# Kernel optimization log

Hardware: AMD Instinct MI355X
Metric: run time of the kernel (lower is better)

Reference implementation:

```python
import jax, jax.numpy as jnp
import numpy as np

NUM_HEADS = 16  # concat repeats the identical head output this many times


def setup_inputs() -> dict:
    key = jax.random.key(0)
    ks = jax.random.split(key, 6)
    B, S, E, D = 4, 4096, 1024, 64  # D = E // NUM_HEADS
    s_in = 1.0 / np.sqrt(E)
    return {
        "x": jax.random.normal(ks[0], (B, S, E), dtype=jnp.float32),
        "Wq": jax.random.normal(ks[1], (E, D), dtype=jnp.float32) * s_in,
        "bq": jnp.zeros((D,), dtype=jnp.float32),
        "Wk": jax.random.normal(ks[2], (E, D), dtype=jnp.float32) * s_in,
        "bk": jnp.zeros((D,), dtype=jnp.float32),
        "Wv": jax.random.normal(ks[3], (E, D), dtype=jnp.float32) * s_in,
        "bv": jnp.zeros((D,), dtype=jnp.float32),
        "Wo": jax.random.normal(ks[4], (E, E), dtype=jnp.float32) * s_in,
        "bo": jnp.zeros((E,), dtype=jnp.float32),
    }


def reference(x, Wq, bq, Wk, bk, Wv, bv, Wo, bo):
    # Single shared projection to head_dim (the torch code projects E -> E//H once).
    q = x @ Wq + bq          # [B,S,D]
    k = x @ Wk + bk          # [B,S,D]
    v = x @ Wv + bv          # [B,S,D]
    d = q.shape[-1]
    scale = 1.0 / jnp.sqrt(jnp.asarray(d, dtype=q.dtype))
    scores = jnp.einsum("bqd,bkd->bqk", q, k) * scale   # [B,S,S]
    attn = jax.nn.softmax(scores, axis=-1)
    ctx = jnp.einsum("bqk,bkd->bqd", attn, v)            # [B,S,D]
    # Every head computes the identical result; concat == tile along features.
    cat = jnp.tile(ctx, (1, 1, NUM_HEADS))               # [B,S,E]
    return cat @ Wo + bo
```

## Files before the change

kernel.cpp:

```cpp
#include <hip/hip_runtime.h>
#include <hip/hip_bf16.h>

#define BB 4
#define SS 4096
#define EE 1024
#define DD 64

typedef unsigned short u16;
typedef unsigned int   u32;
typedef __bf16 bf16_t;
typedef bf16_t bf16x2 __attribute__((ext_vector_type(2)));
typedef bf16_t bf16x8 __attribute__((ext_vector_type(8)));
typedef float  f32x4  __attribute__((ext_vector_type(4)));
typedef u32    u32x4  __attribute__((ext_vector_type(4)));

__device__ __forceinline__ u16 f2bf_hw(float f) {
    bf16_t b = (bf16_t)f;
    u16 u; __builtin_memcpy(&u, &b, 2);
    return u;
}
__device__ __forceinline__ void bfsplit(float v, u16& h, u16& l) {
    bf16_t hb = (bf16_t)v;
    float hf = (float)hb;
    __builtin_memcpy(&h, &hb, 2);
    bf16_t lb = (bf16_t)(v - hf);
    __builtin_memcpy(&l, &lb, 2);
}

__global__ __launch_bounds__(256) void prep_kernel(const float* __restrict__ Wq,
                                                   const float* __restrict__ Wk,
                                                   const float* __restrict__ Wv,
                                                   const float* __restrict__ Wo,
                                                   u16* __restrict__ Wt,
                                                   u16* __restrict__ WoTh,
                                                   u16* __restrict__ WoTl) {
    const int b = blockIdx.x;
    const int tid = threadIdx.x;
    if (b < 768) {
        int t = b * 256 + tid;
        int c = t >> 10, e = t & 1023;
        const float* W = (c < 64) ? Wq : (c < 128) ? Wk : Wv;
        Wt[c * 1024 + e] = f2bf_hw(W[e * 64 + (c & 63)]);
        return;
    }
    const int t = (b - 768) * 256 + tid;
    const int d = t >> 10, e = t & 1023;
    float s = 0.f;
    #pragma unroll
    for (int h = 0; h < 16; h++) s += Wo[(h * 64 + d) * 1024 + e];
    u16 hh, ll;
    bfsplit(s, hh, ll);
    WoTh[e * 64 + d] = hh;
    WoTl[e * 64 + d] = ll;
}

__global__ __launch_bounds__(256) void proj_kernel(const float* __restrict__ x,
                                                   const u16* __restrict__ Wtg,
                                                   const float* __restrict__ bq,
                                                   const float* __restrict__ bk,
                                                   const float* __restrict__ bv,
                                                   u16* __restrict__ Qg,
                                                   u16* __restrict__ Kg,
                                                   u16* __restrict__ Vtg) {
    __shared__ __align__(16) u16 xt[32 * 136];
    __shared__ __align__(16) u16 wts[192 * 136];

    const int tid  = threadIdx.x;
    const int w    = tid >> 6;
    const int lane = tid & 63;
    const int m    = lane & 15;
    const int quad = lane >> 4;
    const int r0   = blockIdx.x * 32;
    const int mt   = w & 1;
    const int ch   = w >> 1;

    f32x4 acc[6];
    #pragma unroll
    for (int i = 0; i < 6; i++) acc[i] = (f32x4){0.f, 0.f, 0.f, 0.f};

    f32x4 xr[4];
    u32x4 wr[12];

    auto preload = [&](int kb) {
        #pragma unroll
        for (int j = 0; j < 2; j++) {
            const int id = tid + j * 256, row = id >> 4, seg = id & 15;
            const float* src = x + (r0 + row) * 1024 + kb * 128 + seg * 8;
            xr[2 * j]     = *(const f32x4*)(src);
            xr[2 * j + 1] = *(const f32x4*)(src + 4);
        }
        #pragma unroll
        for (int j = 0; j < 12; j++) {
            const int id = tid + j * 256, row = id >> 4, seg = id & 15;
            wr[j] = *(const u32x4*)(Wtg + row * 1024 + kb * 128 + seg * 8);
        }
    };
    auto commit = [&]() {
        #pragma unroll
        for (int j = 0; j < 2; j++) {
            const int id = tid + j * 256, row = id >> 4, seg = id & 15;
            bf16x8 v;
            #pragma unroll
            for (int k = 0; k < 4; k++) {
                v[k]     = (bf16_t)xr[2 * j][k];
                v[4 + k] = (bf16_t)xr[2 * j + 1][k];
            }
            *(bf16x8*)(xt + row * 136 + seg * 8) = v;
        }
        #pragma unroll
        for (int j = 0; j < 12; j++) {
            const int id = tid + j * 256, row = id >> 4, seg = id & 15;
            *(u32x4*)(wts + row * 136 + seg * 8) = wr[j];
        }
    };

    preload(0);
    for (int kb = 0; kb < 8; kb++) {
        __syncthreads();
        commit();
        __syncthreads();
        if (kb < 7) preload(kb + 1);
        #pragma unroll
        for (int ks = 0; ks < 4; ks++) {
            bf16x8 a = *(const bf16x8*)(xt + (mt * 16 + m) * 136 + ks * 32 + quad * 8);
            #pragma unroll
            for (int c = 0; c < 6; c++) {
                bf16x8 b = *(const bf16x8*)(wts + (ch * 96 + c * 16 + m) * 136 + ks * 32 + quad * 8);
                acc[c] = __builtin_amdgcn_mfma_f32_16x16x32_bf16(a, b, acc[c], 0, 0, 0);
            }
        }
    }

    const int rbase = r0 + mt * 16 + quad * 4;
    #pragma unroll
    for (int c = 0; c < 6; c++) {
        const int col   = ch * 96 + c * 16 + m;
        const int which = col >> 6;
        const int d     = col & 63;
        const float bias = (which == 0 ? bq : which == 1 ? bk : bv)[d];
        #pragma unroll
        for (int r = 0; r < 4; r++) {
            const int row = rbase + r;
            float v = acc[c][r] + bias;
            if (which == 0) {
                Qg[row * 64 + d] = f2bf_hw(v * 0.125f);
            } else if (which == 1) {
                Kg[row * 64 + d] = f2bf_hw(v);
            } else {
                const int b = row >> 12, s = row & 4095;
                const int sp = (s & ~31) | ((s & 12) << 1) | (s & 3) | ((s >> 2) & 4);
                Vtg[(b * 64 + d) * 4096 + sp] = f2bf_hw(v);
            }
        }
    }
}

#define ATTN_LDS 73728
__global__ __launch_bounds__(512) void attn_kernel(const u16* __restrict__ Qg,
                                                   const u16* __restrict__ Kg,
                                                   const u16* __restrict__ Vtg,
                                                   float* __restrict__ ctxP,
                                                   float* __restrict__ liP) {
    extern __shared__ __align__(16) u16 smem[];

    const int tid  = threadIdx.x;
    const int w    = tid >> 6;
    const int lane = tid & 63;
    const int m    = lane & 15;
    const int quad = lane >> 4;
    const int kg   = w >> 1;
    const int qg   = w & 1;

    const int bi    = blockIdx.x;
    const int khalf = bi & 1;
    const int batch = (bi >> 1) & 3;
    const int qt    = bi >> 3;
    const int qrow0 = batch * 4096 + qt * 64;

    bf16x8 aq[2][2];
    #pragma unroll
    for (int s = 0; s < 2; s++) {
        const int qr = qrow0 + qg * 32 + s * 16 + m;
        aq[s][0] = *(const bf16x8*)(Qg + qr * 64 + quad * 8);
        aq[s][1] = *(const bf16x8*)(Qg + qr * 64 + 32 + quad * 8);
    }

    f32x4 acc[2][4];
    float li[2] = {0.f, 0.f};
    #pragma unroll
    for (int s = 0; s < 2; s++)
        #pragma unroll
        for (int c = 0; c < 4; c++) acc[s][c] = (f32x4){0.f, 0.f, 0.f, 0.f};

    const u16* Kbase = Kg + (batch * 4096 + khalf * 2048) * 64;
    const u16* Vbase = Vtg + batch * 64 * 4096 + khalf * 2048;

    const int krow = qg * 16 + (lane >> 3);
    const int kseg = lane & 7;
    const int kxor = (lane >> 3) & 7;
    const int vrow = qg * 32 + (lane >> 2);
    const int vseg = lane & 3;

    u32x4 kr[2], vr[2];
    auto preload = [&](int it) {
        const int k0 = it * 128 + kg * 32;
        #pragma unroll
        for (int i = 0; i < 2; i++) {
            kr[i] = *(const u32x4*)(Kbase + (k0 + krow + 8 * i) * 64 + kseg * 8);
            vr[i] = *(const u32x4*)(Vbase + (vrow + 16 * i) * 4096 + k0 + vseg * 8);
        }
    };
    auto commit = [&](u16* Kt, u16* Vt) {
        #pragma unroll
        for (int i = 0; i < 2; i++) {
            *(u32x4*)(Kt + (krow + 8 * i) * 64 + ((kseg ^ kxor) * 8)) = kr[i];
            *(u32x4*)(Vt + (vrow + 16 * i) * 40 + vseg * 8) = vr[i];
        }
    };

    const float LOG2E = 1.4426950408889634f;
    const float NC2   = -12.0f * 1.4426950408889634f;

    preload(0);
    {
        u16* base = smem + kg * 4608;
        commit(base, base + 2048);
    }
    __syncthreads();

    for (int it = 0; it < 16; it++) {
        const int cur = it & 1;
        u16* Kt = smem + cur * 18432 + kg * 4608;
        u16* Vt = Kt + 2048;

        if (it < 15) preload(it + 1);

        f32x4 sc[2][2];
        #pragma unroll
        for (int c = 0; c < 2; c++) {
            const int row = c * 16 + m;
            bf16x8 k0f = *(const bf16x8*)(Kt + row * 64 + ((quad ^ (m & 7)) * 8));
            bf16x8 k1f = *(const bf16x8*)(Kt + row * 64 + (((quad | 4) ^ (m & 7)) * 8));
            #pragma unroll
            for (int s = 0; s < 2; s++) {
                f32x4 t = __builtin_amdgcn_mfma_f32_16x16x32_bf16(k0f, aq[s][0], (f32x4){0.f,0.f,0.f,0.f}, 0, 0, 0);
                sc[s][c] = __builtin_amdgcn_mfma_f32_16x16x32_bf16(k1f, aq[s][1], t, 0, 0, 0);
            }
        }

        bf16x8 pa[2];
        #pragma unroll
        for (int s = 0; s < 2; s++) {
            float p[8];
            #pragma unroll
            for (int r = 0; r < 4; r++) {
                p[r]     = __builtin_exp2f(__builtin_fmaf(sc[s][0][r], LOG2E, NC2));
                p[4 + r] = __builtin_exp2f(__builtin_fmaf(sc[s][1][r], LOG2E, NC2));
            }
            li[s] += ((p[0] + p[1]) + (p[2] + p[3])) + ((p[4] + p[5]) + (p[6] + p[7]));
            #pragma unroll
            for (int j = 0; j < 8; j++) pa[s][j] = (bf16_t)p[j];
        }

        #pragma unroll
        for (int c = 0; c < 4; c++) {
            bf16x8 bv = *(const bf16x8*)(Vt + (c * 16 + m) * 40 + quad * 8);
            #pragma unroll
            for (int s = 0; s < 2; s++)
                acc[s][c] = __builtin_amdgcn_mfma_f32_16x16x32_bf16(pa[s], bv, acc[s][c], 0, 0, 0);
        }

        if (it < 15) {
            u16* Kn = smem + (cur ^ 1) * 18432 + kg * 4608;
            commit(Kn, Kn + 2048);
        }
        __syncthreads();
    }

    #pragma unroll
    for (int s = 0; s < 2; s++) {
        float v = li[s];
        v += __shfl_xor(v, 16);
        v += __shfl_xor(v, 32);
        li[s] = v;
    }

    float* mf = (float*)smem;
    float* cb = mf + w * 2208;
    #pragma unroll
    for (int s = 0; s < 2; s++)
        #pragma unroll
        for (int c = 0; c < 4; c++)
            #pragma unroll
            for (int r = 0; r < 4; r++)
                cb[(s * 16 + quad * 4 + r) * 68 + c * 16 + m] = acc[s][c][r];
    if (lane < 16) {
        #pragma unroll
        for (int s = 0; s < 2; s++) cb[2176 + s * 16 + m] = li[s];
    }
    __syncthreads();

    const int q  = tid >> 3;
    const int d0 = (tid & 7) * 8;
    const int qgq = q >> 5;
    const int ql  = q & 31;
    float L = 0.f;
    f32x4 o0 = (f32x4){0.f, 0.f, 0.f, 0.f};
    f32x4 o1 = (f32x4){0.f, 0.f, 0.f, 0.f};
    #pragma unroll
    for (int g = 0; g < 4; g++) {
        const float* c2 = mf + (g * 2 + qgq) * 2208;
        L  += c2[2176 + ql];
        o0 += *(const f32x4*)(c2 + ql * 68 + d0);
        o1 += *(const f32x4*)(c2 + ql * 68 + d0 + 4);
    }
    const int gr = khalf * 16384 + qrow0 + q;
    *(f32x4*)(ctxP + gr * 64 + d0)     = o0;
    *(f32x4*)(ctxP + gr * 64 + d0 + 4) = o1;
    if ((tid & 7) == 0) liP[gr] = L;
}

__global__ __launch_bounds__(256) void out_kernel(const float* __restrict__ ctxP,
                                                  const float* __restrict__ liP,
                                                  const u16* __restrict__ WoTh,
                                                  const u16* __restrict__ WoTl,
                                                  const float* __restrict__ bo,
                                                  float* __restrict__ out) {
    __shared__ __align__(16) u16 ldsH[64 * 72];
    __shared__ __align__(16) u16 ldsL[64 * 72];
    const int tid = threadIdx.x;
    const int r0  = (blockIdx.x >> 2) * 64;
    const int eb  = (blockIdx.x & 3) * 256;

    {
        const int q  = tid >> 2;
        const int dq = (tid & 3) * 16;
        const float inv = 1.0f / (liP[r0 + q] + liP[16384 + r0 + q]);
        const float* A = ctxP + (r0 + q) * 64 + dq;
        const float* B = ctxP + 16384 * 64 + (r0 + q) * 64 + dq;
        #pragma unroll
        for (int i = 0; i < 4; i++) {
            f32x4 a4 = *(const f32x4*)(A + i * 4);
            f32x4 b4 = *(const f32x4*)(B + i * 4);
            f32x4 o  = (a4 + b4) * inv;
            u16 h[4], l[4];
            #pragma unroll
            for (int k = 0; k < 4; k++) bfsplit(o[k], h[k], l[k]);
            u32 h0 = (u32)h[0] | ((u32)h[1] << 16);
            u32 h1 = (u32)h[2] | ((u32)h[3] << 16);
            u32 l0 = (u32)l[0] | ((u32)l[1] << 16);
            u32 l1 = (u32)l[2] | ((u32)l[3] << 16);
            const int off = q * 72 + dq + i * 4;
            *(u32*)(ldsH + off)     = h0;
            *(u32*)(ldsH + off + 2) = h1;
            *(u32*)(ldsL + off)     = l0;
            *(u32*)(ldsL + off + 2) = l1;
        }
    }
    __syncthreads();

    const int w    = tid >> 6;
    const int lane = tid & 63;
    const int m    = lane & 15;
    const int quad = lane >> 4;
    const int wr   = w >> 1;
    const int wc   = w & 1;

    bf16x8 aH[2][2], aL[2][2];
    #pragma unroll
    for (int rs = 0; rs < 2; rs++)
        #pragma unroll
        for (int ks = 0; ks < 2; ks++) {
            const int off = (wr * 32 + rs * 16 + m) * 72 + ks * 32 + quad * 8;
            aH[rs][ks] = *(const bf16x8*)(ldsH + off);
            aL[rs][ks] = *(const bf16x8*)(ldsL + off);
        }

    f32x4 acc[2][8];
    #pragma unroll
    for (int rs = 0; rs < 2; rs++)
        #pragma unroll
        for (int cs = 0; cs < 8; cs++) acc[rs][cs] = (f32x4){0.f, 0.f, 0.f, 0.f};

    #pragma unroll
    for (int cs = 0; cs < 8; cs++) {
        const int e = eb + wc * 128 + cs * 16 + m;
        bf16x8 bh0 = *(const bf16x8*)(WoTh + e * 64 + quad * 8);
        bf16x8 bh1 = *(const bf16x8*)(WoTh + e * 64 + 32 + quad * 8);
        bf16x8 bl0 = *(const bf16x8*)(WoTl + e * 64 + quad * 8);
        bf16x8 bl1 = *(const bf16x8*)(WoTl + e * 64 + 32 + quad * 8);
        #pragma unroll
        for (int rs = 0; rs < 2; rs++) {
            f32x4 t = acc[rs][cs];
            t = __builtin_amdgcn_mfma_f32_16x16x32_bf16(aH[rs][0], bh0, t, 0, 0, 0);
            t = __builtin_amdgcn_mfma_f32_16x16x32_bf16(aH[rs][1], bh1, t, 0, 0, 0);
            t = __builtin_amdgcn_mfma_f32_16x16x32_bf16(aL[rs][0], bh0, t, 0, 0, 0);
            t = __builtin_amdgcn_mfma_f32_16x16x32_bf16(aL[rs][1], bh1, t, 0, 0, 0);
            t = __builtin_amdgcn_mfma_f32_16x16x32_bf16(aH[rs][0], bl0, t, 0, 0, 0);
            t = __builtin_amdgcn_mfma_f32_16x16x32_bf16(aH[rs][1], bl1, t, 0, 0, 0);
            acc[rs][cs] = t;
        }
    }

    #pragma unroll
    for (int cs = 0; cs < 8; cs++) {
        const int e = eb + wc * 128 + cs * 16 + m;
        const float bov = bo[e];
        #pragma unroll
        for (int rs = 0; rs < 2; rs++) {
            const int row = r0 + wr * 32 + rs * 16 + quad * 4;
            #pragma unroll
            for (int r = 0; r < 4; r++)
                out[(row + r) * 1024 + e] = acc[rs][cs][r] + bov;
        }
    }
}

extern "C" void kernel_launch(void* const* d_in, const int* in_sizes, int n_in,
                              void* d_out, int out_size, void* d_ws, size_t ws_size,
                              hipStream_t stream) {
    const float* x  = (const float*)d_in[0];
    const float* Wq = (const float*)d_in[1];
    const float* bq = (const float*)d_in[2];
    const float* Wk = (const float*)d_in[3];
    const float* bk = (const float*)d_in[4];
    const float* Wv = (const float*)d_in[5];
    const float* bv = (const float*)d_in[6];
    const float* Wo = (const float*)d_in[7];
    const float* bo = (const float*)d_in[8];
    float* out = (float*)d_out;

    char* ws = (char*)d_ws;
    u16*   Wt   = (u16*)(ws);
    u16*   WoTh = (u16*)(ws + 393216);
    u16*   WoTl = (u16*)(ws + 524288);
    u16*   Qg   = (u16*)(ws + 655360);
    u16*   Kg   = (u16*)(ws + 2752512);
    u16*   Vtg  = (u16*)(ws + 4849664);
    float* ctxP = (float*)(ws + 6946816);
    float* liP  = (float*)(ws + 15335424);

    (void)hipFuncSetAttribute((const void*)attn_kernel,
                              hipFuncAttributeMaxDynamicSharedMemorySize, ATTN_LDS);

    prep_kernel <<<1024, 256, 0, stream>>>(Wq, Wk, Wv, Wo, Wt, WoTh, WoTl);
    proj_kernel <<<512,  256, 0, stream>>>(x, Wt, bq, bk, bv, Qg, Kg, Vtg);
    attn_kernel <<<512,  512, ATTN_LDS, stream>>>(Qg, Kg, Vtg, ctxP, liP);
    out_kernel  <<<1024, 256, 0, stream>>>(ctxP, liP, WoTh, WoTl, bo, out);
}
```

Measured before the change: 200.6 us.

## Give each wave private K/V LDS tiles, drop per-iteration block barriers, add setprio

```diff
diff --git a/kernel.cpp b/kernel.cpp
--- a/kernel.cpp
+++ b/kernel.cpp
@@ -177,6 +177,9 @@
     const int qt    = bi >> 3;
     const int qrow0 = batch * 4096 + qt * 64;
 
+    u16* Kt = smem + w * 4608;
+    u16* Vt = Kt + 2048;
+
     bf16x8 aq[2][2];
     #pragma unroll
     for (int s = 0; s < 2; s++) {
@@ -195,26 +198,23 @@
     const u16* Kbase = Kg + (batch * 4096 + khalf * 2048) * 64;
     const u16* Vbase = Vtg + batch * 64 * 4096 + khalf * 2048;
 
-    const int krow = qg * 16 + (lane >> 3);
-    const int kseg = lane & 7;
-    const int kxor = (lane >> 3) & 7;
-    const int vrow = qg * 32 + (lane >> 2);
-    const int vseg = lane & 3;
-
-    u32x4 kr[2], vr[2];
+    const int kr8  = lane >> 3, kseg = lane & 7;
+    const int vr4  = lane >> 2, vseg = lane & 3;
+
+    u32x4 kr[4], vr[4];
     auto preload = [&](int it) {
         const int k0 = it * 128 + kg * 32;
         #pragma unroll
-        for (int i = 0; i < 2; i++) {
-            kr[i] = *(const u32x4*)(Kbase + (k0 + krow + 8 * i) * 64 + kseg * 8);
-            vr[i] = *(const u32x4*)(Vbase + (vrow + 16 * i) * 4096 + k0 + vseg * 8);
+        for (int i = 0; i < 4; i++) {
+            kr[i] = *(const u32x4*)(Kbase + (k0 + kr8 + 8 * i) * 64 + kseg * 8);
+            vr[i] = *(const u32x4*)(Vbase + (vr4 + 16 * i) * 4096 + k0 + vseg * 8);
         }
     };
-    auto commit = [&](u16* Kt, u16* Vt) {
-        #pragma unroll
-        for (int i = 0; i < 2; i++) {
-            *(u32x4*)(Kt + (krow + 8 * i) * 64 + ((kseg ^ kxor) * 8)) = kr[i];
-            *(u32x4*)(Vt + (vrow + 16 * i) * 40 + vseg * 8) = vr[i];
+    auto commit = [&]() {
+        #pragma unroll
+        for (int i = 0; i < 4; i++) {
+            *(u32x4*)(Kt + (kr8 + 8 * i) * 64 + ((kseg ^ kr8) * 8)) = kr[i];
+            *(u32x4*)(Vt + (vr4 + 16 * i) * 40 + vseg * 8) = vr[i];
         }
     };
 
@@ -222,20 +222,13 @@
     const float NC2   = -12.0f * 1.4426950408889634f;
 
     preload(0);
-    {
-        u16* base = smem + kg * 4608;
-        commit(base, base + 2048);
-    }
-    __syncthreads();
+    commit();
 
     for (int it = 0; it < 16; it++) {
-        const int cur = it & 1;
-        u16* Kt = smem + cur * 18432 + kg * 4608;
-        u16* Vt = Kt + 2048;
-
         if (it < 15) preload(it + 1);
 
         f32x4 sc[2][2];
+        __builtin_amdgcn_s_setprio(1);
         #pragma unroll
         for (int c = 0; c < 2; c++) {
             const int row = c * 16 + m;
@@ -247,6 +240,7 @@
                 sc[s][c] = __builtin_amdgcn_mfma_f32_16x16x32_bf16(k1f, aq[s][1], t, 0, 0, 0);
             }
         }
+        __builtin_amdgcn_s_setprio(0);
 
         bf16x8 pa[2];
         #pragma unroll
@@ -262,6 +256,7 @@
             for (int j = 0; j < 8; j++) pa[s][j] = (bf16_t)p[j];
         }
 
+        __builtin_amdgcn_s_setprio(1);
         #pragma unroll
         for (int c = 0; c < 4; c++) {
             bf16x8 bv = *(const bf16x8*)(Vt + (c * 16 + m) * 40 + quad * 8);
@@ -269,12 +264,12 @@
             for (int s = 0; s < 2; s++)
                 acc[s][c] = __builtin_amdgcn_mfma_f32_16x16x32_bf16(pa[s], bv, acc[s][c], 0, 0, 0);
         }
+        __builtin_amdgcn_s_setprio(0);
 
         if (it < 15) {
-            u16* Kn = smem + (cur ^ 1) * 18432 + kg * 4608;
-            commit(Kn, Kn + 2048);
-        }
-        __syncthreads();
+            asm volatile("s_waitcnt lgkmcnt(0)" ::: "memory");
+            commit();
+        }
     }
 
     #pragma unroll
@@ -285,6 +280,7 @@
         li[s] = v;
     }
 
+    __syncthreads();
     float* mf = (float*)smem;
     float* cb = mf + w * 2208;
     #pragma unroll
```

Result: no change. 201.6 us (+0.5%).
